# Performance work log

Measured on AMD Instinct MI355X. Metric: run time of the kernel, lower is better.

## Reference

```python
import jax, jax.numpy as jnp
import numpy as np

N_NODES = 100000
N_EDGES = 800000
HIDDEN = 256
BOTTLENECK = 32


def setup_inputs() -> dict:
    key = jax.random.key(0)
    k1, k2, k3, k4 = jax.random.split(key, 4)
    x = jax.random.normal(k1, (N_NODES, HIDDEN), dtype=jnp.float32)
    edge_index = jax.random.randint(k2, (2, N_EDGES), 0, N_NODES, dtype=jnp.int64)
    # PyG GCNConv linear weights, init per module: normal(std=1e-5), zero bias
    W_down = jax.random.normal(k3, (BOTTLENECK, HIDDEN), dtype=jnp.float32) * 1e-5
    b_down = jnp.zeros((BOTTLENECK,), dtype=jnp.float32)
    W_up = jax.random.normal(k4, (HIDDEN, BOTTLENECK), dtype=jnp.float32) * 1e-5
    b_up = jnp.zeros((HIDDEN,), dtype=jnp.float32)
    return {"x": x, "edge_index": edge_index, "W_down": W_down, "b_down": b_down,
            "W_up": W_up, "b_up": b_up}


def reference(x, edge_index, W_down, b_down, W_up, b_up):
    N = x.shape[0]
    loops = jnp.arange(N, dtype=edge_index.dtype)
    # gcn_norm with self-loops (edge weight = 1), symmetric normalization
    row = jnp.concatenate([edge_index[0], loops])  # source nodes
    col = jnp.concatenate([edge_index[1], loops])  # target nodes
    deg = jax.ops.segment_sum(jnp.ones(row.shape[0], dtype=x.dtype), col, num_segments=N)
    dinv = jnp.where(deg > 0, jax.lax.rsqrt(deg), 0.0)
    norm = dinv[row] * dinv[col]  # [E+N]

    def gcn_conv(h, W, b):
        h = h @ W.T                                   # [N, out]
        msgs = h[row] * norm[:, None]                 # gather + weight
        return jax.ops.segment_sum(msgs, col, num_segments=N) + b

    h = jax.nn.relu(gcn_conv(x, W_down, b_down))      # down-proj conv + act
    out = gcn_conv(h, W_up, b_up) + x                 # up-proj conv + skip
    return out
```

## Files before the change

kernel.cpp:

```cpp
#include <hip/hip_runtime.h>
#include <hip/hip_bf16.h>
#include <stdint.h>

#define HID 256
#define BOT 32

typedef short short8 __attribute__((ext_vector_type(8)));
typedef unsigned short ushort8 __attribute__((ext_vector_type(8)));
typedef float floatx4 __attribute__((ext_vector_type(4)));

__device__ __forceinline__ unsigned short f2bu(float f) {
    return (unsigned short)(__float_as_uint(f) >> 16);
}
__device__ __forceinline__ float bu2f(unsigned short u) {
    return __uint_as_float((unsigned int)u << 16);
}
__device__ __forceinline__ short8 pack8(float4 a, float4 b) {
    short8 r;
    r[0] = (short)f2bu(a.x); r[1] = (short)f2bu(a.y);
    r[2] = (short)f2bu(a.z); r[3] = (short)f2bu(a.w);
    r[4] = (short)f2bu(b.x); r[5] = (short)f2bu(b.y);
    r[6] = (short)f2bu(b.z); r[7] = (short)f2bu(b.w);
    return r;
}


__global__ void k_detect(const int* __restrict__ ei, int* __restrict__ flags) {
    int t = threadIdx.x;
    int found = 0;
    for (int i = 0; i < 8; ++i) {
        int slot = 2 * (t * 8 + i) + 1;
        if (ei[slot] != 0) found = 1;
    }
    unsigned long long b = __ballot(found);
    if (t == 0) flags[0] = (b == 0ULL) ? 1 : 0;
}

__global__ void k_deg(const int* __restrict__ ei, int E, int* __restrict__ deg,
                      const int* __restrict__ flags) {
    int mode = flags[0];
    int e = blockIdx.x * blockDim.x + threadIdx.x;
    if (e >= E) return;
    int d = mode ? ei[2 * E + 2 * e] : ei[E + e];
    atomicAdd(deg + d, 1);
}

__global__ __launch_bounds__(256) void k_alloc(const int* __restrict__ deg,
                                               float* __restrict__ dinv,
                                               int* __restrict__ start,
                                               int* __restrict__ cur,
                                               int* __restrict__ cursor, int N) {
    __shared__ int sdata[256];
    __shared__ int sbase;
    int tid = threadIdx.x;
    int i = blockIdx.x * 256 + tid;
    int d = (i < N) ? deg[i] : 0;
    if (i < N) dinv[i] = rsqrtf((float)(d + 1));
    sdata[tid] = d;
    __syncthreads();
    for (int off = 1; off < 256; off <<= 1) {
        int t = (tid >= off) ? sdata[tid - off] : 0;
        __syncthreads();
        sdata[tid] += t;
        __syncthreads();
    }
    if (tid == 0) sbase = atomicAdd(cursor, sdata[255]);
    __syncthreads();
    if (i < N) {
        int st = sbase + sdata[tid] - d;
        start[i] = st;
        cur[i] = st;
    }
}

__global__ void k_fill(const int* __restrict__ ei, int E,
                       const float* __restrict__ dinv,
                       int* __restrict__ cur, int2* __restrict__ srcw,
                       const int* __restrict__ flags) {
    int mode = flags[0];
    int e = blockIdx.x * blockDim.x + threadIdx.x;
    if (e >= E) return;
    int s, d;
    if (mode) { s = ei[2 * e]; d = ei[2 * E + 2 * e]; }
    else      { s = ei[e];     d = ei[E + e]; }
    float w = dinv[s] * dinv[d];
    int slot = atomicAdd(cur + d, 1);
    srcw[slot] = make_int2(s, __float_as_int(w));
}

__global__ __launch_bounds__(256) void k_gemm_down(
    const float* __restrict__ x, const float* __restrict__ Wd,
    unsigned short* __restrict__ P, int N, int nwaves)
{
    int wid  = (blockIdx.x * 256 + threadIdx.x) >> 6;
    int lane = threadIdx.x & 63;
    int m = lane & 15, q = lane >> 4;

    short8 bfr[2][8];
    #pragma unroll
    for (int jt = 0; jt < 2; ++jt) {
        const float4* wr = (const float4*)(Wd + (size_t)(jt * 16 + m) * HID);
        #pragma unroll
        for (int ks = 0; ks < 8; ++ks) {
            int c = (ks * 32 + q * 8) >> 2;
            bfr[jt][ks] = pack8(wr[c], wr[c + 1]);
        }
    }

    int tiles = (N + 15) >> 4;
    for (int t = wid; t < tiles; t += nwaves) {
        int n0 = t << 4;
        int row = n0 + m; if (row >= N) row = N - 1;
        const float4* xr = (const float4*)(x + (size_t)row * HID);
        floatx4 acc0 = {0.f, 0.f, 0.f, 0.f};
        floatx4 acc1 = {0.f, 0.f, 0.f, 0.f};
        #pragma unroll
        for (int ks = 0; ks < 8; ++ks) {
            int c = (ks * 32 + q * 8) >> 2;
            short8 af = pack8(xr[c], xr[c + 1]);
            acc0 = __builtin_amdgcn_mfma_f32_16x16x32_bf16(bfr[0][ks], af, acc0, 0, 0, 0);
            acc1 = __builtin_amdgcn_mfma_f32_16x16x32_bf16(bfr[1][ks], af, acc1, 0, 0, 0);
        }
        if (n0 + m < N) {
            unsigned int* pr = (unsigned int*)(P + (size_t)(n0 + m) * BOT);
            uint2 v0, v1;
            v0.x = (unsigned int)f2bu(acc0[0]) | ((unsigned int)f2bu(acc0[1]) << 16);
            v0.y = (unsigned int)f2bu(acc0[2]) | ((unsigned int)f2bu(acc0[3]) << 16);
            v1.x = (unsigned int)f2bu(acc1[0]) | ((unsigned int)f2bu(acc1[1]) << 16);
            v1.y = (unsigned int)f2bu(acc1[2]) | ((unsigned int)f2bu(acc1[3]) << 16);
            *(uint2*)(pr + q * 2)     = v0;
            *(uint2*)(pr + 8 + q * 2) = v1;
        }
    }
}

__global__ __launch_bounds__(256) void k_gather(
    const unsigned short* __restrict__ feat, const float* __restrict__ dinv,
    const int* __restrict__ start, const int* __restrict__ endp,
    const int2* __restrict__ srcw, const float* __restrict__ bias,
    unsigned short* __restrict__ dst, int N, int relu_bias)
{
    int t = blockIdx.x * 256 + threadIdx.x;
    int n = t >> 2, tg = t & 3, jq = tg * 8;
    if (n >= N) return;
    float di = dinv[n];
    float w0 = di * di;
    float acc[8];
    ushort8 sv = *(const ushort8*)(feat + (size_t)n * BOT + jq);
    #pragma unroll
    for (int i = 0; i < 8; ++i) acc[i] = w0 * bu2f(sv[i]);
    int k = start[n], en = endp[n];
    for (; k < en; k += 4) {
        int kk = k + tg;
        int2 p = make_int2(0, 0);
        if (kk < en) p = srcw[kk];
        #pragma unroll
        for (int e = 0; e < 4; ++e) {
            int   src = __shfl(p.x, e, 4);
            float w   = __uint_as_float((unsigned int)__shfl(p.y, e, 4));
            ushort8 f = *(const ushort8*)(feat + (size_t)src * BOT + jq);
            #pragma unroll
            for (int i = 0; i < 8; ++i) acc[i] += w * bu2f(f[i]);
        }
    }
    if (relu_bias) {
        #pragma unroll
        for (int i = 0; i < 8; ++i) {
            float a = acc[i] + bias[jq + i];
            acc[i] = a > 0.f ? a : 0.f;
        }
    }
    ushort8 o;
    #pragma unroll
    for (int i = 0; i < 8; ++i) o[i] = f2bu(acc[i]);
    *(ushort8*)(dst + (size_t)n * BOT + jq) = o;
}

__global__ __launch_bounds__(256) void k_out(
    const unsigned short* __restrict__ A2, const float* __restrict__ x,
    const float* __restrict__ Wup, const float* __restrict__ bup,
    float* __restrict__ out, int N)
{
    int gw   = (blockIdx.x * 256 + threadIdx.x) >> 6;
    int lane = threadIdx.x & 63;
    int m = lane & 15, q = lane >> 4;
    int tiles = (N + 15) >> 4;
    int t = gw >> 1, h = gw & 1;
    if (t >= tiles) return;

    int n0 = t << 4;
    int arow = n0 + m; if (arow >= N) arow = N - 1;
    short8 af = *(const short8*)(A2 + (size_t)arow * BOT + q * 8);
    const float4* xrow = (const float4*)(x + (size_t)arow * HID);
    floatx4* orow = (floatx4*)(out + (size_t)arow * HID);
    bool ok = (n0 + m) < N;
    #pragma unroll
    for (int i = 0; i < 8; ++i) {
        int ft = h * 8 + i;
        const float4* wr = (const float4*)(Wup + (size_t)(ft * 16 + m) * BOT);
        short8 bfr = pack8(wr[q * 2], wr[q * 2 + 1]);
        floatx4 acc = {0.f, 0.f, 0.f, 0.f};
        acc = __builtin_amdgcn_mfma_f32_16x16x32_bf16(bfr, af, acc, 0, 0, 0);
        if (ok) {
            int c = ft * 4 + q;
            float4 xv = xrow[c];
            float4 bb = *(const float4*)(bup + ft * 16 + q * 4);
            floatx4 res;
            res[0] = acc[0] + bb.x + xv.x;
            res[1] = acc[1] + bb.y + xv.y;
            res[2] = acc[2] + bb.z + xv.z;
            res[3] = acc[3] + bb.w + xv.w;
            __builtin_nontemporal_store(res, &orow[c]);
        }
    }
}

extern "C" void kernel_launch(void* const* d_in, const int* in_sizes, int n_in,
                              void* d_out, int out_size, void* d_ws, size_t ws_size,
                              hipStream_t stream) {
    const float* x  = (const float*)d_in[0];
    const int*   ei = (const int*)d_in[1];
    const float* Wd = (const float*)d_in[2];
    const float* bd = (const float*)d_in[3];
    const float* Wu = (const float*)d_in[4];
    const float* bu = (const float*)d_in[5];
    float* out = (float*)d_out;

    int N = in_sizes[0] / HID;
    int E = in_sizes[1] / 2;

    char* ws = (char*)d_ws;
    int*   flags = (int*)ws;
    int*   deg   = (int*)(ws + 16);
    float* dinv  = (float*)(ws + 16 + (size_t)N * 4);
    int*   startp= (int*)(ws + 16 + (size_t)N * 8);
    int*   curp  = (int*)(ws + 16 + (size_t)N * 12);
    int2*  srcw  = (int2*)(ws + 16 + (size_t)N * 16);
    unsigned short* P  = (unsigned short*)(ws + 16 + (size_t)N * 16 + (size_t)E * 8);
    unsigned short* A1 = (unsigned short*)(ws + 16 + (size_t)N * 16 + (size_t)E * 8 + (size_t)N * 64);

    (void)hipMemsetAsync(ws, 0, 16 + (size_t)N * 4, stream);
    k_detect<<<1, 64, 0, stream>>>(ei, flags);
    k_deg<<<(E + 255) / 256, 256, 0, stream>>>(ei, E, deg, flags);

    k_alloc<<<(N + 255) / 256, 256, 0, stream>>>(deg, dinv, startp, curp, flags + 1, N);
    k_fill<<<(E + 255) / 256, 256, 0, stream>>>(ei, E, dinv, curp, srcw, flags);

    int tiles = (N + 15) / 16;
    int gblocks = (tiles + 3) / 4;
    k_gemm_down<<<gblocks, 256, 0, stream>>>(x, Wd, P, N, gblocks * 4);
    int gthreads = N * 4;
    k_gather<<<(gthreads + 255) / 256, 256, 0, stream>>>(P, dinv, startp, curp, srcw, bd, A1, N, 1);

    k_gather<<<(gthreads + 255) / 256, 256, 0, stream>>>(A1, dinv, startp, curp, srcw, bd, P, N, 0);

    int oblocks = (tiles * 2 + 3) / 4;
    k_out<<<oblocks, 256, 0, stream>>>(P, x, Wu, bu, out, N);
}
```

Measured before the change: 360.1 us.

## Vectorize edge loads, unroll gather loop, and use nontemporal loads for x

```diff
diff --git a/kernel.cpp b/kernel.cpp
--- a/kernel.cpp
+++ b/kernel.cpp
@@ -23,6 +23,15 @@
     r[6] = (short)f2bu(b.z); r[7] = (short)f2bu(b.w);
     return r;
 }
+__device__ __forceinline__ short8 pack8v(floatx4 a, floatx4 b) {
+    short8 r;
+    #pragma unroll
+    for (int i = 0; i < 4; ++i) {
+        r[i]     = (short)f2bu(a[i]);
+        r[4 + i] = (short)f2bu(b[i]);
+    }
+    return r;
+}
 
 
 __global__ void k_detect(const int* __restrict__ ei, int* __restrict__ flags) {
@@ -39,10 +48,29 @@
 __global__ void k_deg(const int* __restrict__ ei, int E, int* __restrict__ deg,
                       const int* __restrict__ flags) {
     int mode = flags[0];
-    int e = blockIdx.x * blockDim.x + threadIdx.x;
-    if (e >= E) return;
-    int d = mode ? ei[2 * E + 2 * e] : ei[E + e];
-    atomicAdd(deg + d, 1);
+    int t = blockIdx.x * blockDim.x + threadIdx.x;
+    int e0 = t * 4;
+    if (e0 >= E) return;
+    int d0, d1, d2, d3;
+    if (e0 + 4 <= E) {
+        if (mode) {
+            const int4* p = (const int4*)(ei + 2 * (size_t)E + 2 * e0);
+            int4 a = p[0], b = p[1];
+            d0 = a.x; d1 = a.z; d2 = b.x; d3 = b.z;
+        } else {
+            int4 a = *(const int4*)(ei + (size_t)E + e0);
+            d0 = a.x; d1 = a.y; d2 = a.z; d3 = a.w;
+        }
+        atomicAdd(deg + d0, 1);
+        atomicAdd(deg + d1, 1);
+        atomicAdd(deg + d2, 1);
+        atomicAdd(deg + d3, 1);
+    } else {
+        for (int e = e0; e < E; ++e) {
+            int d = mode ? ei[2 * (size_t)E + 2 * e] : ei[(size_t)E + e];
+            atomicAdd(deg + d, 1);
+        }
+    }
 }
 
 __global__ __launch_bounds__(256) void k_alloc(const int* __restrict__ deg,
@@ -78,14 +106,39 @@
                        int* __restrict__ cur, int2* __restrict__ srcw,
                        const int* __restrict__ flags) {
     int mode = flags[0];
-    int e = blockIdx.x * blockDim.x + threadIdx.x;
-    if (e >= E) return;
-    int s, d;
-    if (mode) { s = ei[2 * e]; d = ei[2 * E + 2 * e]; }
-    else      { s = ei[e];     d = ei[E + e]; }
-    float w = dinv[s] * dinv[d];
-    int slot = atomicAdd(cur + d, 1);
-    srcw[slot] = make_int2(s, __float_as_int(w));
+    int t = blockIdx.x * blockDim.x + threadIdx.x;
+    int e0 = t * 4;
+    if (e0 >= E) return;
+    int s[4], d[4];
+    if (e0 + 4 <= E) {
+        if (mode) {
+            const int4* ps = (const int4*)(ei + 2 * (size_t)e0);
+            const int4* pd = (const int4*)(ei + 2 * (size_t)E + 2 * e0);
+            int4 sa = ps[0], sb = ps[1], da = pd[0], db = pd[1];
+            s[0] = sa.x; s[1] = sa.z; s[2] = sb.x; s[3] = sb.z;
+            d[0] = da.x; d[1] = da.z; d[2] = db.x; d[3] = db.z;
+        } else {
+            int4 sa = *(const int4*)(ei + (size_t)e0);
+            int4 da = *(const int4*)(ei + (size_t)E + e0);
+            s[0] = sa.x; s[1] = sa.y; s[2] = sa.z; s[3] = sa.w;
+            d[0] = da.x; d[1] = da.y; d[2] = da.z; d[3] = da.w;
+        }
+        #pragma unroll
+        for (int u = 0; u < 4; ++u) {
+            float w = dinv[s[u]] * dinv[d[u]];
+            int slot = atomicAdd(cur + d[u], 1);
+            srcw[slot] = make_int2(s[u], __float_as_int(w));
+        }
+    } else {
+        for (int e = e0; e < E; ++e) {
+            int ss, dd;
+            if (mode) { ss = ei[2 * (size_t)e]; dd = ei[2 * (size_t)E + 2 * e]; }
+            else      { ss = ei[(size_t)e];     dd = ei[(size_t)E + e]; }
+            float w = dinv[ss] * dinv[dd];
+            int slot = atomicAdd(cur + dd, 1);
+            srcw[slot] = make_int2(ss, __float_as_int(w));
+        }
+    }
 }
 
 __global__ __launch_bounds__(256) void k_gemm_down(
@@ -111,13 +164,15 @@
     for (int t = wid; t < tiles; t += nwaves) {
         int n0 = t << 4;
         int row = n0 + m; if (row >= N) row = N - 1;
-        const float4* xr = (const float4*)(x + (size_t)row * HID);
+        const floatx4* xr = (const floatx4*)(x + (size_t)row * HID);
         floatx4 acc0 = {0.f, 0.f, 0.f, 0.f};
         floatx4 acc1 = {0.f, 0.f, 0.f, 0.f};
         #pragma unroll
         for (int ks = 0; ks < 8; ++ks) {
             int c = (ks * 32 + q * 8) >> 2;
-            short8 af = pack8(xr[c], xr[c + 1]);
+            floatx4 va = __builtin_nontemporal_load(xr + c);
+            floatx4 vb = __builtin_nontemporal_load(xr + c + 1);
+            short8 af = pack8v(va, vb);
             acc0 = __builtin_amdgcn_mfma_f32_16x16x32_bf16(bfr[0][ks], af, acc0, 0, 0, 0);
             acc1 = __builtin_amdgcn_mfma_f32_16x16x32_bf16(bfr[1][ks], af, acc1, 0, 0, 0);
         }
@@ -141,7 +196,7 @@
     unsigned short* __restrict__ dst, int N, int relu_bias)
 {
     int t = blockIdx.x * 256 + threadIdx.x;
-    int n = t >> 2, tg = t & 3, jq = tg * 8;
+    int n = t >> 2, jq = (t & 3) * 8;
     if (n >= N) return;
     float di = dinv[n];
     float w0 = di * di;
@@ -150,18 +205,26 @@
     #pragma unroll
     for (int i = 0; i < 8; ++i) acc[i] = w0 * bu2f(sv[i]);
     int k = start[n], en = endp[n];
-    for (; k < en; k += 4) {
-        int kk = k + tg;
-        int2 p = make_int2(0, 0);
-        if (kk < en) p = srcw[kk];
-        #pragma unroll
-        for (int e = 0; e < 4; ++e) {
-            int   src = __shfl(p.x, e, 4);
-            float w   = __uint_as_float((unsigned int)__shfl(p.y, e, 4));
-            ushort8 f = *(const ushort8*)(feat + (size_t)src * BOT + jq);
+    while (k < en) {
+        int2 p[8];
+        #pragma unroll
+        for (int u = 0; u < 8; ++u) {
+            int kk = k + u;
+            int safe = kk < en ? kk : en - 1;
+            p[u] = srcw[safe];
+            if (kk >= en) p[u].y = 0;
+        }
+        ushort8 f[8];
+        #pragma unroll
+        for (int u = 0; u < 8; ++u)
+            f[u] = *(const ushort8*)(feat + (size_t)p[u].x * BOT + jq);
+        #pragma unroll
+        for (int u = 0; u < 8; ++u) {
+            float w = __int_as_float(p[u].y);
             #pragma unroll
-            for (int i = 0; i < 8; ++i) acc[i] += w * bu2f(f[i]);
-        }
+            for (int i = 0; i < 8; ++i) acc[i] += w * bu2f(f[u][i]);
+        }
+        k += 8;
     }
     if (relu_bias) {
         #pragma unroll
@@ -191,7 +254,7 @@
     int n0 = t << 4;
     int arow = n0 + m; if (arow >= N) arow = N - 1;
     short8 af = *(const short8*)(A2 + (size_t)arow * BOT + q * 8);
-    const float4* xrow = (const float4*)(x + (size_t)arow * HID);
+    const floatx4* xrow = (const floatx4*)(x + (size_t)arow * HID);
     floatx4* orow = (floatx4*)(out + (size_t)arow * HID);
     bool ok = (n0 + m) < N;
     #pragma unroll
@@ -203,13 +266,13 @@
         acc = __builtin_amdgcn_mfma_f32_16x16x32_bf16(bfr, af, acc, 0, 0, 0);
         if (ok) {
             int c = ft * 4 + q;
-            float4 xv = xrow[c];
+            floatx4 xv = __builtin_nontemporal_load(xrow + c);
             float4 bb = *(const float4*)(bup + ft * 16 + q * 4);
             floatx4 res;
-            res[0] = acc[0] + bb.x + xv.x;
-            res[1] = acc[1] + bb.y + xv.y;
-            res[2] = acc[2] + bb.z + xv.z;
-            res[3] = acc[3] + bb.w + xv.w;
+            res[0] = acc[0] + bb.x + xv[0];
+            res[1] = acc[1] + bb.y + xv[1];
+            res[2] = acc[2] + bb.z + xv[2];
+            res[3] = acc[3] + bb.w + xv[3];
             __builtin_nontemporal_store(res, &orow[c]);
         }
     }
@@ -241,10 +304,11 @@
 
     (void)hipMemsetAsync(ws, 0, 16 + (size_t)N * 4, stream);
     k_detect<<<1, 64, 0, stream>>>(ei, flags);
-    k_deg<<<(E + 255) / 256, 256, 0, stream>>>(ei, E, deg, flags);
+    int ethreads = (E + 3) / 4;
+    k_deg<<<(ethreads + 255) / 256, 256, 0, stream>>>(ei, E, deg, flags);
 
     k_alloc<<<(N + 255) / 256, 256, 0, stream>>>(deg, dinv, startp, curp, flags + 1, N);
-    k_fill<<<(E + 255) / 256, 256, 0, stream>>>(ei, E, dinv, curp, srcw, flags);
+    k_fill<<<(ethreads + 255) / 256, 256, 0, stream>>>(ei, E, dinv, curp, srcw, flags);
 
     int tiles = (N + 15) / 16;
     int gblocks = (tiles + 3) / 4;
```

Measured after the change: 412.9 us. 14.7% more time.
